# Performance work log

Measured on AMD Instinct MI355X. Metric: run time of the kernel, lower is better.

Reference implementation:

```python
import jax, jax.numpy as jnp
import numpy as np

N_NODES = 100_000
N_EDGES = 1_000_000
LATENT = 64
HID_ATOM = 256
HID_BOND = 256
RBF_DIM = 32
RBF_DMAX = 10.0
N_ATOM_TYPES = 10
N_CHARGES = 6
N_BOND_ORDERS = 5


def setup_inputs() -> dict:
    key = jax.random.key(0)
    ks = jax.random.split(key, 12)
    positions = jax.random.normal(ks[0], (N_NODES, 3), dtype=jnp.float32) * 5.0
    quantized = jax.random.normal(ks[1], (N_NODES, LATENT), dtype=jnp.float32)
    pair_indices = jax.random.randint(ks[2], (N_EDGES, 2), 0, N_NODES, dtype=jnp.int64)
    s = 0.05
    return {
        "positions": positions,
        "quantized": quantized,
        "pair_indices": pair_indices,
        "aW1": jax.random.normal(ks[3], (LATENT, HID_ATOM), jnp.float32) * s,
        "ab1": jnp.zeros((HID_ATOM,), jnp.float32),
        "aW2": jax.random.normal(ks[4], (HID_ATOM, N_ATOM_TYPES + N_CHARGES), jnp.float32) * s,
        "ab2": jnp.zeros((N_ATOM_TYPES + N_CHARGES,), jnp.float32),
        "bW1": jax.random.normal(ks[5], (LATENT + RBF_DIM, HID_BOND), jnp.float32) * s,
        "bb1": jnp.zeros((HID_BOND,), jnp.float32),
        "bW2": jax.random.normal(ks[6], (HID_BOND, N_BOND_ORDERS), jnp.float32) * s,
        "bb2": jnp.zeros((N_BOND_ORDERS,), jnp.float32),
    }


def _norm_no_nan(x, eps=1e-8):
    # L2 norm over last axis, clamped to avoid NaN gradients at 0
    return jnp.sqrt(jnp.maximum(jnp.sum(x * x, axis=-1), eps))


def _rbf(D, D_min=0.0, D_max=RBF_DMAX, D_count=RBF_DIM):
    mu = jnp.linspace(D_min, D_max, D_count, dtype=D.dtype)  # [D_count]
    sigma = (D_max - D_min) / D_count
    z = (D[..., None] - mu) / sigma
    return jnp.exp(-z * z)  # [E, D_count]


def reference(positions, quantized, pair_indices, aW1, ab1, aW2, ab2, bW1, bb1, bW2, bb2):
    src = pair_indices[:, 0]
    dst = pair_indices[:, 1]
    # pairwise distances -> RBF expansion
    x_i = positions[src]            # [E, 3]
    x_j = positions[dst]
    dists = _rbf(_norm_no_nan(x_i - x_j))  # [E, rbf_dim]
    # atom decoder (per node)
    h = jax.nn.relu(quantized @ aW1 + ab1)
    scalar_logits = h @ aW2 + ab2
    atom_type_logits = scalar_logits[:, :N_ATOM_TYPES]
    atom_charge_logits = scalar_logits[:, N_ATOM_TYPES:]
    # bond decoder (per edge): gathered latent sum concat RBF
    pair_feats = quantized[src] + quantized[dst]           # [E, latent]
    combined = jnp.concatenate([pair_feats, dists], axis=1)  # [E, latent+rbf]
    hb = jax.nn.relu(combined @ bW1 + bb1)
    bond_order_logits = hb @ bW2 + bb2
    return (atom_type_logits, atom_charge_logits, bond_order_logits)
```

## Files before the change

kernel.cpp:

```cpp
#include <hip/hip_runtime.h>
#include <hip/hip_bf16.h>

typedef __bf16 bf16x8 __attribute__((ext_vector_type(8)));
typedef __bf16 bf16x4 __attribute__((ext_vector_type(4)));
typedef float  f32x4  __attribute__((ext_vector_type(4)));
typedef short  s16x4  __attribute__((ext_vector_type(4)));

#define N_NODES 100000
#define N_EDGES 1000000
#define LATENT  64
#define HID     256
#define RBF_DIM 32
#define NTYPES  10
#define NCHG    6
#define NBOND   5

#define ATOM_TILES (N_NODES / 32)
#define ANBLK 512

#define ETILE  32
#define ETILES (N_EDGES / ETILE)
#define ENBLK  768

static __device__ __forceinline__ f32x4 mfma16(bf16x4 a, bf16x4 b, f32x4 c) {
#if __has_builtin(__builtin_amdgcn_mfma_f32_16x16x16bf16_1k)
    s16x4 ai = __builtin_bit_cast(s16x4, a);
    s16x4 bi = __builtin_bit_cast(s16x4, b);
    return __builtin_amdgcn_mfma_f32_16x16x16bf16_1k(ai, bi, c, 0, 0, 0);
#else
    asm volatile("s_nop 1\n\t"
                 "v_mfma_f32_16x16x16_bf16 %0, %1, %2, %0\n\t"
                 "s_nop 7\n\ts_nop 7"
                 : "+v"(c) : "v"(a), "v"(b));
    return c;
#endif
}

__global__ __launch_bounds__(256) void dist_kernel(
    const float* __restrict__ pos, const int* __restrict__ pair,
    float* __restrict__ dist)
{
    const int e = blockIdx.x * 256 + threadIdx.x;
    if (e >= N_EDGES) return;
    const int2 pr = ((const int2*)pair)[e];
    const float dx = pos[(unsigned)pr.x * 3u]      - pos[(unsigned)pr.y * 3u];
    const float dy = pos[(unsigned)pr.x * 3u + 1u] - pos[(unsigned)pr.y * 3u + 1u];
    const float dz = pos[(unsigned)pr.x * 3u + 2u] - pos[(unsigned)pr.y * 3u + 2u];
    dist[e] = sqrtf(fmaxf(dx * dx + dy * dy + dz * dz, 1e-8f));
}

struct __align__(16) ASmem {
    __bf16 qs[32][72];
    __bf16 hsE[32][264];
    float  red[4][2][4][64];
};

template<bool EMIT_QB>
__global__ __launch_bounds__(256, 2) void atom_kernel(
    const float* __restrict__ q,   const float* __restrict__ aW1,
    const float* __restrict__ ab1, const float* __restrict__ aW2,
    const float* __restrict__ ab2, float* __restrict__ outA,
    float* __restrict__ outB,      __bf16* __restrict__ qb)
{
    __shared__ ASmem sm;
    const int t    = threadIdx.x;
    const int w    = t >> 6;
    const int lane = t & 63;
    const int l15  = lane & 15;
    const int hi   = lane >> 4;
    const int wcol = w * 64;

    bf16x8 aw1f[2][4];
    #pragma unroll
    for (int kb = 0; kb < 2; ++kb)
        #pragma unroll
        for (int nt = 0; nt < 4; ++nt) {
            const int nn = wcol + nt * 16 + l15;
            const int k0 = kb * 32 + hi * 8;
            bf16x8 v;
            #pragma unroll
            for (int j = 0; j < 8; ++j) v[j] = (__bf16)aW1[(k0 + j) * HID + nn];
            aw1f[kb][nt] = v;
        }
    bf16x8 aw2f[2];
    #pragma unroll
    for (int kk = 0; kk < 2; ++kk) {
        const int k0 = (w * 2 + kk) * 32 + hi * 8;
        bf16x8 v;
        #pragma unroll
        for (int j = 0; j < 8; ++j) v[j] = (__bf16)aW2[(k0 + j) * 16 + l15];
        aw2f[kk] = v;
    }
    float4 b1v[4];
    #pragma unroll
    for (int nt = 0; nt < 4; ++nt)
        b1v[nt] = *(const float4*)(&ab1[wcol + nt * 16 + hi * 4]);

    const int m_st = t >> 3;
    const int p_st = t & 7;

    for (int tile = blockIdx.x; tile < ATOM_TILES; tile += ANBLK) {
        const int node0 = tile * 32;
        {
            const float* qr = q + (size_t)(node0 + m_st) * 64 + p_st * 8;
            const float4 a0 = *(const float4*)(qr);
            const float4 a1 = *(const float4*)(qr + 4);
            bf16x8 v;
            v[0] = (__bf16)a0.x; v[1] = (__bf16)a0.y; v[2] = (__bf16)a0.z; v[3] = (__bf16)a0.w;
            v[4] = (__bf16)a1.x; v[5] = (__bf16)a1.y; v[6] = (__bf16)a1.z; v[7] = (__bf16)a1.w;
            *(bf16x8*)(&sm.qs[m_st][p_st * 8]) = v;
            if constexpr (EMIT_QB)
                *(bf16x8*)(qb + (size_t)(node0 + m_st) * 64 + p_st * 8) = v;
        }
        __syncthreads();

        f32x4 acc[2][4];
        #pragma unroll
        for (int mt = 0; mt < 2; ++mt)
            #pragma unroll
            for (int nt = 0; nt < 4; ++nt)
                #pragma unroll
                for (int r = 0; r < 4; ++r)
                    acc[mt][nt][r] = ((const float*)&b1v[nt])[r];

        #pragma unroll
        for (int kb = 0; kb < 2; ++kb)
            #pragma unroll
            for (int mt = 0; mt < 2; ++mt) {
                const bf16x8 bq = *(const bf16x8*)((const char*)&sm.qs[0][0]
                                   + (mt * 16 + l15) * 144 + kb * 64 + hi * 16);
                #pragma unroll
                for (int nt = 0; nt < 4; ++nt)
                    acc[mt][nt] = __builtin_amdgcn_mfma_f32_16x16x32_bf16(
                        aw1f[kb][nt], bq, acc[mt][nt], 0, 0, 0);
            }

        #pragma unroll
        for (int mt = 0; mt < 2; ++mt)
            #pragma unroll
            for (int nt = 0; nt < 4; ++nt) {
                bf16x4 hv;
                #pragma unroll
                for (int r = 0; r < 4; ++r)
                    hv[r] = (__bf16)fmaxf(acc[mt][nt][r], 0.f);
                *(bf16x4*)(&sm.hsE[mt * 16 + l15][wcol + nt * 16 + hi * 4]) = hv;
            }
        __syncthreads();

        f32x4 acc2[2];
        {
            f32x4 z = {0.f, 0.f, 0.f, 0.f};
            acc2[0] = z; acc2[1] = z;
        }
        #pragma unroll
        for (int mt = 0; mt < 2; ++mt)
            #pragma unroll
            for (int kk = 0; kk < 2; ++kk) {
                const int kb = w * 2 + kk;
                const bf16x8 af = *(const bf16x8*)((const char*)&sm.hsE[0][0]
                                   + (mt * 16 + l15) * 528 + kb * 64 + hi * 16);
                acc2[mt] = __builtin_amdgcn_mfma_f32_16x16x32_bf16(
                    af, aw2f[kk], acc2[mt], 0, 0, 0);
            }
        #pragma unroll
        for (int mt = 0; mt < 2; ++mt)
            #pragma unroll
            for (int r = 0; r < 4; ++r)
                sm.red[w][mt][r][lane] = acc2[mt][r];
        __syncthreads();

        {
            const int o  = t & 15;
            const int m0 = t >> 4;
            #pragma unroll
            for (int half = 0; half < 2; ++half) {
                const int m  = m0 + half * 16;
                const int mt = m >> 4, rr = m & 15;
                const int hh = rr >> 2, r = rr & 3;
                float s = ab2[o];
                #pragma unroll
                for (int ww = 0; ww < 4; ++ww) s += sm.red[ww][mt][r][hh * 16 + o];
                const int node = node0 + m;
                if (o < NTYPES) outA[node * NTYPES + o] = s;
                else            outB[node * NCHG + (o - NTYPES)] = s;
            }
        }
        __syncthreads();
    }
}

struct __align__(16) ESmem {
    __bf16 comb[2][ETILE][168];
    float  red[2][4][2][4][64];
};

__device__ __forceinline__ void bar_lgkm() {
    asm volatile("s_waitcnt lgkmcnt(0)" ::: "memory");
    __builtin_amdgcn_s_barrier();
}

template<bool USEBF>
__global__ __launch_bounds__(256, 3) void edge_kernel(
    const float* __restrict__ pos, const float* __restrict__ qf,
    const __bf16* __restrict__ qb, const float* __restrict__ dist,
    const int* __restrict__ pair,
    const float* __restrict__ bW1, const float* __restrict__ bb1,
    const float* __restrict__ bW2, const float* __restrict__ bb2,
    float* __restrict__ outC)
{
    __shared__ ESmem sm;
    const int t    = threadIdx.x;
    const int w    = t >> 6;
    const int lane = t & 63;
    const int l15  = lane & 15;
    const int hi   = lane >> 4;
    const int hid0 = w * 64;

    bf16x8 bw1f[3][4];
    #pragma unroll
    for (int kb = 0; kb < 3; ++kb)
        #pragma unroll
        for (int nt = 0; nt < 4; ++nt) {
            const int nn = hid0 + nt * 16 + l15;
            const int k0 = kb * 32 + hi * 8;
            bf16x8 v;
            #pragma unroll
            for (int j = 0; j < 8; ++j) v[j] = (__bf16)bW1[(k0 + j) * HID + nn];
            bw1f[kb][nt] = v;
        }
    bf16x4 w2f[4];
    #pragma unroll
    for (int nt = 0; nt < 4; ++nt) {
        bf16x4 v;
        #pragma unroll
        for (int j = 0; j < 4; ++j)
            v[j] = (l15 < NBOND)
                 ? (__bf16)bW2[(hid0 + nt * 16 + hi * 4 + j) * NBOND + l15]
                 : (__bf16)0.f;
        w2f[nt] = v;
    }
    float4 b1v[4];
    #pragma unroll
    for (int nt = 0; nt < 4; ++nt)
        b1v[nt] = *(const float4*)(&bb1[hid0 + nt * 16 + hi * 4]);

    const int e_loc = t >> 3;
    const int p     = t & 7;

    const int ep_m  = t / 5, ep_o = t % 5;
    const int ep_mt = ep_m >> 4;
    const int ep_hh = (ep_m & 15) >> 2, ep_r = ep_m & 3;

    int tile = blockIdx.x;
    bf16x8 gs, gd;
    float  Dv;
    float4 fs0, fs1, fd0, fd1;
    float  ps0, ps1, ps2, pd0, pd1, pd2;

    #define GATHER(pN, tg)                                                        \
        if constexpr (USEBF) {                                                    \
            gs = *(const bf16x8*)(qb + ((unsigned)(pN).x * 64u + (unsigned)(p*8)));\
            gd = *(const bf16x8*)(qb + ((unsigned)(pN).y * 64u + (unsigned)(p*8)));\
            Dv = dist[(size_t)(tg) * ETILE + e_loc];                              \
        } else {                                                                  \
            fs0 = *(const float4*)(qf + ((unsigned)(pN).x * 64u + (unsigned)(p*8)));     \
            fs1 = *(const float4*)(qf + ((unsigned)(pN).x * 64u + (unsigned)(p*8) + 4u));\
            fd0 = *(const float4*)(qf + ((unsigned)(pN).y * 64u + (unsigned)(p*8)));     \
            fd1 = *(const float4*)(qf + ((unsigned)(pN).y * 64u + (unsigned)(p*8) + 4u));\
            ps0 = pos[(unsigned)(pN).x * 3u];  ps1 = pos[(unsigned)(pN).x * 3u + 1u];    \
            ps2 = pos[(unsigned)(pN).x * 3u + 2u];                                \
            pd0 = pos[(unsigned)(pN).y * 3u];  pd1 = pos[(unsigned)(pN).y * 3u + 1u];    \
            pd2 = pos[(unsigned)(pN).y * 3u + 2u];                                \
        }

    #define STAGE(buf)                                                            \
        {                                                                         \
            char* rowp = (char*)&sm.comb[buf][0][0] + e_loc * 336;                \
            float D;                                                              \
            if constexpr (USEBF) {                                                \
                *(bf16x8*)(rowp + p * 16)       = gs;                             \
                *(bf16x8*)(rowp + 128 + p * 16) = gd;                             \
                D = Dv;                                                           \
            } else {                                                              \
                bf16x8 vs, vd;                                                    \
                vs[0] = (__bf16)fs0.x; vs[1] = (__bf16)fs0.y;                     \
                vs[2] = (__bf16)fs0.z; vs[3] = (__bf16)fs0.w;                     \
                vs[4] = (__bf16)fs1.x; vs[5] = (__bf16)fs1.y;                     \
                vs[6] = (__bf16)fs1.z; vs[7] = (__bf16)fs1.w;                     \
                vd[0] = (__bf16)fd0.x; vd[1] = (__bf16)fd0.y;                     \
                vd[2] = (__bf16)fd0.z; vd[3] = (__bf16)fd0.w;                     \
                vd[4] = (__bf16)fd1.x; vd[5] = (__bf16)fd1.y;                     \
                vd[6] = (__bf16)fd1.z; vd[7] = (__bf16)fd1.w;                     \
                *(bf16x8*)(rowp + p * 16)       = vs;                             \
                *(bf16x8*)(rowp + 128 + p * 16) = vd;                             \
                const float dx = ps0 - pd0, dy = ps1 - pd1, dz = ps2 - pd2;       \
                D = sqrtf(fmaxf(dx * dx + dy * dy + dz * dz, 1e-8f));             \
            }                                                                     \
            bf16x4 rv;                                                            \
            _Pragma("unroll")                                                     \
            for (int j = 0; j < 4; ++j) {                                         \
                const float mu = (float)(p * 4 + j) * (10.0f / 31.0f);            \
                const float z  = (D - mu) * 3.2f;                                 \
                rv[j] = (__bf16)__expf(-z * z);                                   \
            }                                                                     \
            *(bf16x4*)(rowp + 256 + p * 8) = rv;                                  \
        }

    int  tgA = tile;
    int2 pA  = ((const int2*)pair)[(size_t)tile * ETILE + e_loc];
    GATHER(pA, tgA);
    tgA = (tile + ENBLK < ETILES) ? tile + ENBLK : 0;
    pA  = ((const int2*)pair)[(size_t)tgA * ETILE + e_loc];
    STAGE(0);
    GATHER(pA, tgA);
    tgA = (tile + 2 * ENBLK < ETILES) ? tile + 2 * ENBLK : 0;
    pA  = ((const int2*)pair)[(size_t)tgA * ETILE + e_loc];
    bar_lgkm();

    int cur = 0;
    int e0_prev = -1;

    for (; tile < ETILES; tile += ENBLK) {
        const int e0 = tile * ETILE;

        if (e0_prev >= 0 && t < 160) {
            float s = bb2[ep_o];
            #pragma unroll
            for (int ww = 0; ww < 4; ++ww)
                s += sm.red[cur ^ 1][ww][ep_mt][ep_r][ep_hh * 16 + ep_o];
            outC[(size_t)(e0_prev + ep_m) * NBOND + ep_o] = s;
        }

        STAGE(cur ^ 1);

        GATHER(pA, tgA);
        tgA = (tile + 3 * ENBLK < ETILES) ? tile + 3 * ENBLK : 0;
        pA  = ((const int2*)pair)[(size_t)tgA * ETILE + e_loc];

        f32x4 acc[2][4];
        #pragma unroll
        for (int mt = 0; mt < 2; ++mt)
            #pragma unroll
            for (int nt = 0; nt < 4; ++nt)
                #pragma unroll
                for (int r = 0; r < 4; ++r)
                    acc[mt][nt][r] = ((const float*)&b1v[nt])[r];

        #pragma unroll
        for (int kb = 0; kb < 5; ++kb) {
            const int kbu = (kb < 2) ? kb : ((kb < 4) ? kb - 2 : 2);
            #pragma unroll
            for (int mt = 0; mt < 2; ++mt) {
                const bf16x8 bf = *(const bf16x8*)((const char*)&sm.comb[cur][0][0]
                                   + (mt * 16 + l15) * 336 + kb * 64 + hi * 16);
                #pragma unroll
                for (int nt = 0; nt < 4; ++nt)
                    acc[mt][nt] = __builtin_amdgcn_mfma_f32_16x16x32_bf16(
                        bw1f[kbu][nt], bf, acc[mt][nt], 0, 0, 0);
            }
        }

        {
            f32x4 acc2[2];
            {
                f32x4 z = {0.f, 0.f, 0.f, 0.f};
                acc2[0] = z; acc2[1] = z;
            }
            #pragma unroll
            for (int mt = 0; mt < 2; ++mt)
                #pragma unroll
                for (int nt = 0; nt < 4; ++nt) {
                    bf16x4 hv;
                    #pragma unroll
                    for (int r = 0; r < 4; ++r)
                        hv[r] = (__bf16)fmaxf(acc[mt][nt][r], 0.f);
                    acc2[mt] = mfma16(hv, w2f[nt], acc2[mt]);
                }
            #pragma unroll
            for (int mt = 0; mt < 2; ++mt)
                #pragma unroll
                for (int r = 0; r < 4; ++r)
                    sm.red[cur][w][mt][r][lane] = acc2[mt][r];
        }

        e0_prev = e0;
        bar_lgkm();
        cur ^= 1;
    }

    if (e0_prev >= 0 && t < 160) {
        float s = bb2[ep_o];
        #pragma unroll
        for (int ww = 0; ww < 4; ++ww)
            s += sm.red[cur ^ 1][ww][ep_mt][ep_r][ep_hh * 16 + ep_o];
        outC[(size_t)(e0_prev + ep_m) * NBOND + ep_o] = s;
    }
    #undef GATHER
    #undef STAGE
}

extern "C" void kernel_launch(void* const* d_in, const int* in_sizes, int n_in,
                              void* d_out, int out_size, void* d_ws, size_t ws_size,
                              hipStream_t stream)
{
    const float* pos = (const float*)d_in[0];
    const float* q   = (const float*)d_in[1];
    const int*   pair= (const int*)  d_in[2];
    const float* aW1 = (const float*)d_in[3];
    const float* ab1 = (const float*)d_in[4];
    const float* aW2 = (const float*)d_in[5];
    const float* ab2 = (const float*)d_in[6];
    const float* bW1 = (const float*)d_in[7];
    const float* bb1 = (const float*)d_in[8];
    const float* bW2 = (const float*)d_in[9];
    const float* bb2 = (const float*)d_in[10];

    float* out  = (float*)d_out;
    float* outA = out;
    float* outB = out + (size_t)N_NODES * NTYPES;
    float* outC = out + (size_t)N_NODES * (NTYPES + NCHG);

    const size_t qb_bytes   = (size_t)N_NODES * LATENT * sizeof(__bf16);
    const size_t dist_bytes = (size_t)N_EDGES * sizeof(float);
    const bool use_bf = (ws_size >= qb_bytes + dist_bytes);
    __bf16* qb   = (__bf16*)d_ws;
    float*  dist = (float*)((char*)d_ws + qb_bytes);

    if (use_bf) {
        hipLaunchKernelGGL(dist_kernel, dim3((N_EDGES + 255) / 256), dim3(256),
                           0, stream, pos, pair, dist);
        hipLaunchKernelGGL(atom_kernel<true>, dim3(ANBLK), dim3(256), 0, stream,
                           q, aW1, ab1, aW2, ab2, outA, outB, qb);
        hipLaunchKernelGGL(edge_kernel<true>, dim3(ENBLK), dim3(256), 0, stream,
                           pos, q, qb, dist, pair, bW1, bb1, bW2, bb2, outC);
    } else {
        hipLaunchKernelGGL(atom_kernel<false>, dim3(ANBLK), dim3(256), 0, stream,
                           q, aW1, ab1, aW2, ab2, outA, outB, qb);
        hipLaunchKernelGGL(edge_kernel<false>, dim3(ENBLK), dim3(256), 0, stream,
                           pos, q, qb, dist, pair, bW1, bb1, bW2, bb2, outC);
    }
}
```

Measured before the change: 121.4 us.

## Pre-sum gathered latents before GEMM and double edge tile size

Edge latents are now summed (src+dst) at staging time, so the first bond GEMM runs K=96 (64 summed latent + 32 RBF) instead of K=160, using three MFMA k-blocks rather than five. The edge tile grows from 32 to 64 edges, processed in two passes of 32, and the second-layer reduction buffer keeps only the 5 useful output columns. This cuts MFMA work and LDS traffic per edge, but summing in bf16 slightly changes rounding. The larger tile also raises register pressure and the amount of work done per barrier.

```diff
diff --git a/kernel.cpp b/kernel.cpp
--- a/kernel.cpp
+++ b/kernel.cpp
@@ -18,7 +18,7 @@
 #define ATOM_TILES (N_NODES / 32)
 #define ANBLK 512
 
-#define ETILE  32
+#define ETILE  64
 #define ETILES (N_EDGES / ETILE)
 #define ENBLK  768
 
@@ -190,8 +190,8 @@
 }
 
 struct __align__(16) ESmem {
-    __bf16 comb[2][ETILE][168];
-    float  red[2][4][2][4][64];
+    __bf16 comb[2][ETILE][104];
+    float  red[2][4][4][4][4][6];
 };
 
 __device__ __forceinline__ void bar_lgkm() {
@@ -244,66 +244,66 @@
     for (int nt = 0; nt < 4; ++nt)
         b1v[nt] = *(const float4*)(&bb1[hid0 + nt * 16 + hi * 4]);
 
-    const int e_loc = t >> 3;
-    const int p     = t & 7;
-
-    const int ep_m  = t / 5, ep_o = t % 5;
-    const int ep_mt = ep_m >> 4;
-    const int ep_hh = (ep_m & 15) >> 2, ep_r = ep_m & 3;
+    const int e_loc = t >> 2;
+    const int p     = t & 3;
+
+    const int ep_m0 = t / 5, ep_o = t % 5;
 
     int tile = blockIdx.x;
-    bf16x8 gs, gd;
+    bf16x8 gs0, gs1, gd0, gd1;
     float  Dv;
-    float4 fs0, fs1, fd0, fd1;
-    float  ps0, ps1, ps2, pd0, pd1, pd2;
+    float4 fs0, fs1, fs2, fs3, fd0, fd1, fd2, fd3;
 
     #define GATHER(pN, tg)                                                        \
         if constexpr (USEBF) {                                                    \
-            gs = *(const bf16x8*)(qb + ((unsigned)(pN).x * 64u + (unsigned)(p*8)));\
-            gd = *(const bf16x8*)(qb + ((unsigned)(pN).y * 64u + (unsigned)(p*8)));\
-            Dv = dist[(size_t)(tg) * ETILE + e_loc];                              \
+            const __bf16* qs_ = qb + ((unsigned)(pN).x * 64u + (unsigned)(p*16)); \
+            const __bf16* qd_ = qb + ((unsigned)(pN).y * 64u + (unsigned)(p*16)); \
+            gs0 = *(const bf16x8*)(qs_);     gs1 = *(const bf16x8*)(qs_ + 8);     \
+            gd0 = *(const bf16x8*)(qd_);     gd1 = *(const bf16x8*)(qd_ + 8);     \
+            Dv  = dist[(size_t)(tg) * ETILE + e_loc];                             \
         } else {                                                                  \
-            fs0 = *(const float4*)(qf + ((unsigned)(pN).x * 64u + (unsigned)(p*8)));     \
-            fs1 = *(const float4*)(qf + ((unsigned)(pN).x * 64u + (unsigned)(p*8) + 4u));\
-            fd0 = *(const float4*)(qf + ((unsigned)(pN).y * 64u + (unsigned)(p*8)));     \
-            fd1 = *(const float4*)(qf + ((unsigned)(pN).y * 64u + (unsigned)(p*8) + 4u));\
-            ps0 = pos[(unsigned)(pN).x * 3u];  ps1 = pos[(unsigned)(pN).x * 3u + 1u];    \
-            ps2 = pos[(unsigned)(pN).x * 3u + 2u];                                \
-            pd0 = pos[(unsigned)(pN).y * 3u];  pd1 = pos[(unsigned)(pN).y * 3u + 1u];    \
-            pd2 = pos[(unsigned)(pN).y * 3u + 2u];                                \
+            const float* qs_ = qf + ((unsigned)(pN).x * 64u + (unsigned)(p*16));  \
+            const float* qd_ = qf + ((unsigned)(pN).y * 64u + (unsigned)(p*16));  \
+            fs0 = *(const float4*)(qs_);      fs1 = *(const float4*)(qs_ + 4);    \
+            fs2 = *(const float4*)(qs_ + 8);  fs3 = *(const float4*)(qs_ + 12);   \
+            fd0 = *(const float4*)(qd_);      fd1 = *(const float4*)(qd_ + 4);    \
+            fd2 = *(const float4*)(qd_ + 8);  fd3 = *(const float4*)(qd_ + 12);   \
+            Dv  = dist[(size_t)(tg) * ETILE + e_loc];                             \
         }
 
     #define STAGE(buf)                                                            \
         {                                                                         \
-            char* rowp = (char*)&sm.comb[buf][0][0] + e_loc * 336;                \
-            float D;                                                              \
+            char* rowp = (char*)&sm.comb[buf][0][0] + e_loc * 208;                \
             if constexpr (USEBF) {                                                \
-                *(bf16x8*)(rowp + p * 16)       = gs;                             \
-                *(bf16x8*)(rowp + 128 + p * 16) = gd;                             \
-                D = Dv;                                                           \
+                bf16x8 c0, c1;                                                    \
+                _Pragma("unroll")                                                 \
+                for (int j = 0; j < 8; ++j) {                                     \
+                    c0[j] = (__bf16)((float)gs0[j] + (float)gd0[j]);              \
+                    c1[j] = (__bf16)((float)gs1[j] + (float)gd1[j]);              \
+                }                                                                 \
+                *(bf16x8*)(rowp + p * 32)      = c0;                              \
+                *(bf16x8*)(rowp + p * 32 + 16) = c1;                              \
             } else {                                                              \
-                bf16x8 vs, vd;                                                    \
-                vs[0] = (__bf16)fs0.x; vs[1] = (__bf16)fs0.y;                     \
-                vs[2] = (__bf16)fs0.z; vs[3] = (__bf16)fs0.w;                     \
-                vs[4] = (__bf16)fs1.x; vs[5] = (__bf16)fs1.y;                     \
-                vs[6] = (__bf16)fs1.z; vs[7] = (__bf16)fs1.w;                     \
-                vd[0] = (__bf16)fd0.x; vd[1] = (__bf16)fd0.y;                     \
-                vd[2] = (__bf16)fd0.z; vd[3] = (__bf16)fd0.w;                     \
-                vd[4] = (__bf16)fd1.x; vd[5] = (__bf16)fd1.y;                     \
-                vd[6] = (__bf16)fd1.z; vd[7] = (__bf16)fd1.w;                     \
-                *(bf16x8*)(rowp + p * 16)       = vs;                             \
-                *(bf16x8*)(rowp + 128 + p * 16) = vd;                             \
-                const float dx = ps0 - pd0, dy = ps1 - pd1, dz = ps2 - pd2;       \
-                D = sqrtf(fmaxf(dx * dx + dy * dy + dz * dz, 1e-8f));             \
+                bf16x8 c0, c1;                                                    \
+                c0[0] = (__bf16)(fs0.x + fd0.x); c0[1] = (__bf16)(fs0.y + fd0.y); \
+                c0[2] = (__bf16)(fs0.z + fd0.z); c0[3] = (__bf16)(fs0.w + fd0.w); \
+                c0[4] = (__bf16)(fs1.x + fd1.x); c0[5] = (__bf16)(fs1.y + fd1.y); \
+                c0[6] = (__bf16)(fs1.z + fd1.z); c0[7] = (__bf16)(fs1.w + fd1.w); \
+                c1[0] = (__bf16)(fs2.x + fd2.x); c1[1] = (__bf16)(fs2.y + fd2.y); \
+                c1[2] = (__bf16)(fs2.z + fd2.z); c1[3] = (__bf16)(fs2.w + fd2.w); \
+                c1[4] = (__bf16)(fs3.x + fd3.x); c1[5] = (__bf16)(fs3.y + fd3.y); \
+                c1[6] = (__bf16)(fs3.z + fd3.z); c1[7] = (__bf16)(fs3.w + fd3.w); \
+                *(bf16x8*)(rowp + p * 32)      = c0;                              \
+                *(bf16x8*)(rowp + p * 32 + 16) = c1;                              \
             }                                                                     \
-            bf16x4 rv;                                                            \
+            bf16x8 rv;                                                            \
             _Pragma("unroll")                                                     \
-            for (int j = 0; j < 4; ++j) {                                         \
-                const float mu = (float)(p * 4 + j) * (10.0f / 31.0f);            \
-                const float z  = (D - mu) * 3.2f;                                 \
+            for (int j = 0; j < 8; ++j) {                                         \
+                const float mu = (float)(p * 8 + j) * (10.0f / 31.0f);            \
+                const float z  = (Dv - mu) * 3.2f;                                \
                 rv[j] = (__bf16)__expf(-z * z);                                   \
             }                                                                     \
-            *(bf16x4*)(rowp + 256 + p * 8) = rv;                                  \
+            *(bf16x8*)(rowp + 128 + p * 16) = rv;                                 \
         }
 
     int  tgA = tile;
@@ -324,11 +324,17 @@
         const int e0 = tile * ETILE;
 
         if (e0_prev >= 0 && t < 160) {
-            float s = bb2[ep_o];
-            #pragma unroll
-            for (int ww = 0; ww < 4; ++ww)
-                s += sm.red[cur ^ 1][ww][ep_mt][ep_r][ep_hh * 16 + ep_o];
-            outC[(size_t)(e0_prev + ep_m) * NBOND + ep_o] = s;
+            #pragma unroll
+            for (int half = 0; half < 2; ++half) {
+                const int m  = ep_m0 + half * 32;
+                const int mt = m >> 4, row = m & 15;
+                const int hh = row >> 2, r = row & 3;
+                float s = bb2[ep_o];
+                #pragma unroll
+                for (int ww = 0; ww < 4; ++ww)
+                    s += sm.red[cur ^ 1][ww][mt][hh][r][ep_o];
+                outC[(size_t)(e0_prev + m) * NBOND + ep_o] = s;
+            }
         }
 
         STAGE(cur ^ 1);
@@ -337,50 +343,47 @@
         tgA = (tile + 3 * ENBLK < ETILES) ? tile + 3 * ENBLK : 0;
         pA  = ((const int2*)pair)[(size_t)tgA * ETILE + e_loc];
 
-        f32x4 acc[2][4];
-        #pragma unroll
-        for (int mt = 0; mt < 2; ++mt)
-            #pragma unroll
-            for (int nt = 0; nt < 4; ++nt)
-                #pragma unroll
-                for (int r = 0; r < 4; ++r)
-                    acc[mt][nt][r] = ((const float*)&b1v[nt])[r];
-
-        #pragma unroll
-        for (int kb = 0; kb < 5; ++kb) {
-            const int kbu = (kb < 2) ? kb : ((kb < 4) ? kb - 2 : 2);
-            #pragma unroll
-            for (int mt = 0; mt < 2; ++mt) {
-                const bf16x8 bf = *(const bf16x8*)((const char*)&sm.comb[cur][0][0]
-                                   + (mt * 16 + l15) * 336 + kb * 64 + hi * 16);
+        #pragma unroll
+        for (int pass = 0; pass < 2; ++pass) {
+            f32x4 acc[2][4];
+            #pragma unroll
+            for (int mti = 0; mti < 2; ++mti)
                 #pragma unroll
                 for (int nt = 0; nt < 4; ++nt)
-                    acc[mt][nt] = __builtin_amdgcn_mfma_f32_16x16x32_bf16(
-                        bw1f[kbu][nt], bf, acc[mt][nt], 0, 0, 0);
-            }
-        }
-
-        {
-            f32x4 acc2[2];
-            {
-                f32x4 z = {0.f, 0.f, 0.f, 0.f};
-                acc2[0] = z; acc2[1] = z;
-            }
-            #pragma unroll
-            for (int mt = 0; mt < 2; ++mt)
+                    #pragma unroll
+                    for (int r = 0; r < 4; ++r)
+                        acc[mti][nt][r] = ((const float*)&b1v[nt])[r];
+
+            #pragma unroll
+            for (int kb = 0; kb < 3; ++kb)
+                #pragma unroll
+                for (int mti = 0; mti < 2; ++mti) {
+                    const int erow = (pass * 2 + mti) * 16 + l15;
+                    const bf16x8 bf = *(const bf16x8*)((const char*)&sm.comb[cur][0][0]
+                                       + erow * 208 + kb * 64 + hi * 16);
+                    #pragma unroll
+                    for (int nt = 0; nt < 4; ++nt)
+                        acc[mti][nt] = __builtin_amdgcn_mfma_f32_16x16x32_bf16(
+                            bw1f[kb][nt], bf, acc[mti][nt], 0, 0, 0);
+                }
+
+            #pragma unroll
+            for (int mti = 0; mti < 2; ++mti) {
+                f32x4 acc2 = {0.f, 0.f, 0.f, 0.f};
                 #pragma unroll
                 for (int nt = 0; nt < 4; ++nt) {
                     bf16x4 hv;
                     #pragma unroll
                     for (int r = 0; r < 4; ++r)
-                        hv[r] = (__bf16)fmaxf(acc[mt][nt][r], 0.f);
-                    acc2[mt] = mfma16(hv, w2f[nt], acc2[mt]);
+                        hv[r] = (__bf16)fmaxf(acc[mti][nt][r], 0.f);
+                    acc2 = mfma16(hv, w2f[nt], acc2);
                 }
-            #pragma unroll
-            for (int mt = 0; mt < 2; ++mt)
-                #pragma unroll
-                for (int r = 0; r < 4; ++r)
-                    sm.red[cur][w][mt][r][lane] = acc2[mt][r];
+                if (l15 < NBOND) {
+                    #pragma unroll
+                    for (int r = 0; r < 4; ++r)
+                        sm.red[cur][w][pass * 2 + mti][hi][r][l15] = acc2[r];
+                }
+            }
         }
 
         e0_prev = e0;
@@ -389,11 +392,17 @@
     }
 
     if (e0_prev >= 0 && t < 160) {
-        float s = bb2[ep_o];
-        #pragma unroll
-        for (int ww = 0; ww < 4; ++ww)
-            s += sm.red[cur ^ 1][ww][ep_mt][ep_r][ep_hh * 16 + ep_o];
-        outC[(size_t)(e0_prev + ep_m) * NBOND + ep_o] = s;
+        #pragma unroll
+        for (int half = 0; half < 2; ++half) {
+            const int m  = ep_m0 + half * 32;
+            const int mt = m >> 4, row = m & 15;
+            const int hh = row >> 2, r = row & 3;
+            float s = bb2[ep_o];
+            #pragma unroll
+            for (int ww = 0; ww < 4; ++ww)
+                s += sm.red[cur ^ 1][ww][mt][hh][r][ep_o];
+            outC[(size_t)(e0_prev + m) * NBOND + ep_o] = s;
+        }
     }
     #undef GATHER
     #undef STAGE
@@ -423,10 +432,10 @@
     const size_t qb_bytes   = (size_t)N_NODES * LATENT * sizeof(__bf16);
     const size_t dist_bytes = (size_t)N_EDGES * sizeof(float);
     const bool use_bf = (ws_size >= qb_bytes + dist_bytes);
-    __bf16* qb   = (__bf16*)d_ws;
-    float*  dist = (float*)((char*)d_ws + qb_bytes);
 
     if (use_bf) {
+        __bf16* qb   = (__bf16*)d_ws;
+        float*  dist = (float*)((char*)d_ws + qb_bytes);
         hipLaunchKernelGGL(dist_kernel, dim3((N_EDGES + 255) / 256), dim3(256),
                            0, stream, pos, pair, dist);
         hipLaunchKernelGGL(atom_kernel<true>, dim3(ANBLK), dim3(256), 0, stream,
@@ -434,9 +443,13 @@
         hipLaunchKernelGGL(edge_kernel<true>, dim3(ENBLK), dim3(256), 0, stream,
                            pos, q, qb, dist, pair, bW1, bb1, bW2, bb2, outC);
     } else {
+        float* dist = (float*)d_ws;
+        hipLaunchKernelGGL(dist_kernel, dim3((N_EDGES + 255) / 256), dim3(256),
+                           0, stream, pos, pair, dist);
         hipLaunchKernelGGL(atom_kernel<false>, dim3(ANBLK), dim3(256), 0, stream,
-                           q, aW1, ab1, aW2, ab2, outA, outB, qb);
+                           q, aW1, ab1, aW2, ab2, outA, outB, (__bf16*)nullptr);
         hipLaunchKernelGGL(edge_kernel<false>, dim3(ENBLK), dim3(256), 0, stream,
-                           pos, q, qb, dist, pair, bW1, bb1, bW2, bb2, outC);
-    }
-}
+                           pos, q, (const __bf16*)nullptr, dist, pair,
+                           bW1, bb1, bW2, bb2, outC);
+    }
+}
```

After: 107.6 us. 1.13x faster.
